# Performance work log

Hardware: AMD Instinct MI355X
Metric: run time of the kernel (lower is better)

## Reference

```python
import jax, jax.numpy as jnp
import numpy as np

C, H, V, N, T = 1024, 256, 10000, 16, 256


def setup_inputs() -> dict:
    key = jax.random.key(0)
    ks = jax.random.split(key, 16)
    s = 1.0 / np.sqrt(H)
    rn = lambda k, shape, sc: (jax.random.normal(k, shape, dtype=jnp.float32) * sc)
    d = {}
    d["text"] = jax.random.randint(ks[0], (N, T), 0, V)
    d["start_emb"] = rn(ks[1], (C, H), 1.0)
    d["sw1"] = rn(ks[2], (H, H), s); d["sb1"] = jnp.zeros((H,), jnp.float32)
    d["sw2"] = rn(ks[3], (H, H), s); d["sb2"] = jnp.zeros((H,), jnp.float32)
    d["sw3"] = rn(ks[4], (H, 1), s); d["sb3"] = jnp.zeros((1,), jnp.float32)
    d["state_emb"] = rn(ks[5], (C, H), 1.0)
    d["tw1"] = rn(ks[6], (H, H), s); d["tb1"] = jnp.zeros((H,), jnp.float32)
    d["tw2"] = rn(ks[7], (H, H), s); d["tb2"] = jnp.zeros((H,), jnp.float32)
    d["tw3"] = rn(ks[8], (H, C), s); d["tb3"] = jnp.zeros((C,), jnp.float32)
    d["pre_emb"] = rn(ks[9], (C, H), 1.0)
    d["ew1"] = rn(ks[10], (H, H), s); d["eb1"] = jnp.zeros((H,), jnp.float32)
    d["ew2"] = rn(ks[11], (H, H), s); d["eb2"] = jnp.zeros((H,), jnp.float32)
    d["ew3"] = rn(ks[12], (H, V), s); d["eb3"] = jnp.zeros((V,), jnp.float32)
    return d


def _res(x, w1, b1, w2, b2):
    # ResidualLayerOld: relu(lin2(relu(lin1(x)))) + x
    return jax.nn.relu(jax.nn.relu(x @ w1 + b1) @ w2 + b2) + x


def reference(text, start_emb, sw1, sb1, sw2, sb2, sw3, sb3,
              state_emb, tw1, tb1, tw2, tb2, tw3, tb3,
              pre_emb, ew1, eb1, ew2, eb2, ew3, eb3):
    # start: [C] log p(z_0)
    start = jax.nn.log_softmax((_res(start_emb, sw1, sb1, sw2, sb2) @ sw3 + sb3)[:, 0])
    # transition: log_softmax over next state, then permute -> [next, prev]
    trans = jax.nn.log_softmax(_res(state_emb, tw1, tb1, tw2, tb2) @ tw3 + tb3, axis=-1).T
    # emission: log_softmax over vocab, permute -> [V, C]
    emit = jax.nn.log_softmax(_res(pre_emb, ew1, eb1, ew2, eb2) @ ew3 + eb3, axis=-1).T

    obs = emit[text]                      # [N, T, C] log p(x_t | z_t=c)
    alpha0 = start[None, :] + obs[:, 0]   # [N, C]

    def step(alpha, e_t):
        # log-semiring matvec: alpha'[n,j] = logsumexp_i alpha[n,i] + trans[j,i]
        a = jax.scipy.special.logsumexp(alpha[:, None, :] + trans[None, :, :], axis=-1) + e_t
        return a, None

    alpha, _ = jax.lax.scan(step, alpha0, jnp.swapaxes(obs, 0, 1)[1:])
    # evidence: logsumexp over final states, summed over batch (full lengths)
    return jax.scipy.special.logsumexp(alpha, axis=-1).sum()
```

## Files before the change

kernel.cpp:

```cpp
#include <hip/hip_runtime.h>
#include <hip/hip_bf16.h>
#include <cstddef>

#define CC 1024
#define HH 256
#define VV 10000
#define NN 16
#define TT 256
#define NB 16

typedef __attribute__((ext_vector_type(8))) short s8b;
typedef __attribute__((ext_vector_type(4))) float f32x4;
typedef __attribute__((ext_vector_type(4))) unsigned int u32x4;

__device__ __forceinline__ unsigned short f2bf(float f) {
    unsigned int b = __builtin_bit_cast(unsigned int, f);
    b += 0x7FFFu + ((b >> 16) & 1u);
    return (unsigned short)(b >> 16);
}
__device__ __forceinline__ float bf2f(unsigned short u) {
    return __builtin_bit_cast(float, ((unsigned int)u) << 16);
}

struct ResArgs { const float *x, *w1, *b1, *w2, *b2; float* o; };
struct ResArgs3 { ResArgs a[3]; };

__global__ __launch_bounds__(256) void k_res(ResArgs3 A)
{
    ResArgs R = A.a[blockIdx.y];
    const int r0 = blockIdx.x * 16;
    const int th = threadIdx.x;
    __shared__ float xs[256][24];
    __shared__ float hs[256][24];
    #pragma unroll
    for (int k = 0; k < 16; k++) xs[th][k] = R.x[(size_t)(r0 + k) * HH + th];
    __syncthreads();
    float acc[16];
    float b1v = R.b1[th];
    #pragma unroll
    for (int r = 0; r < 16; r++) acc[r] = b1v;
    for (int h = 0; h < HH; h++) {
        float w = R.w1[(size_t)h * HH + th];
        #pragma unroll
        for (int r = 0; r < 16; r++) acc[r] = fmaf(xs[h][r], w, acc[r]);
    }
    #pragma unroll
    for (int r = 0; r < 16; r++) hs[th][r] = fmaxf(acc[r], 0.f);
    __syncthreads();
    float b2v = R.b2[th];
    #pragma unroll
    for (int r = 0; r < 16; r++) acc[r] = b2v;
    for (int h = 0; h < HH; h++) {
        float w = R.w2[(size_t)h * HH + th];
        #pragma unroll
        for (int r = 0; r < 16; r++) acc[r] = fmaf(hs[h][r], w, acc[r]);
    }
    #pragma unroll
    for (int r = 0; r < 16; r++) {
        size_t idx = (size_t)(r0 + r) * HH + th;
        R.o[idx] = fmaxf(acc[r], 0.f) + R.x[idx];
    }
}

__global__ __launch_bounds__(256) void k_slog(const float* __restrict__ res_s,
                                              const float* __restrict__ sw3,
                                              const float* __restrict__ sb3,
                                              float* __restrict__ slog)
{
    __shared__ float wv[256];
    const int th = threadIdx.x;
    const int c = blockIdx.x * 256 + th;
    wv[th] = sw3[th];
    __syncthreads();
    const float* row = res_s + (size_t)c * HH;
    float acc = 0.f;
    for (int h = 0; h < HH; h++) acc = fmaf(row[h], wv[h], acc);
    slog[c] = acc + sb3[0];
}

__global__ __launch_bounds__(256) void k_pt(const float* __restrict__ res_t,
                                            const float* __restrict__ tw3,
                                            const float* __restrict__ tb3,
                                            unsigned short* __restrict__ PB)
{
    const int r0 = blockIdx.x * 4;
    const int th = threadIdx.x;
    __shared__ float rs[4][256];
    __shared__ float sred[256];
    for (int k = 0; k < 4; k++) rs[k][th] = res_t[(size_t)(r0 + k) * HH + th];
    __syncthreads();
    float acc[4][4];
    #pragma unroll
    for (int r = 0; r < 4; r++)
        #pragma unroll
        for (int q = 0; q < 4; q++) acc[r][q] = tb3[th + q * 256];
    for (int h = 0; h < HH; h++) {
        float w0 = tw3[(size_t)h * CC + th];
        float w1 = tw3[(size_t)h * CC + th + 256];
        float w2 = tw3[(size_t)h * CC + th + 512];
        float w3 = tw3[(size_t)h * CC + th + 768];
        #pragma unroll
        for (int r = 0; r < 4; r++) {
            float xv = rs[r][h];
            acc[r][0] = fmaf(xv, w0, acc[r][0]);
            acc[r][1] = fmaf(xv, w1, acc[r][1]);
            acc[r][2] = fmaf(xv, w2, acc[r][2]);
            acc[r][3] = fmaf(xv, w3, acc[r][3]);
        }
    }
    for (int r = 0; r < 4; r++) {
        float m = fmaxf(fmaxf(acc[r][0], acc[r][1]), fmaxf(acc[r][2], acc[r][3]));
        sred[th] = m; __syncthreads();
        for (int off = 128; off > 0; off >>= 1) { if (th < off) sred[th] = fmaxf(sred[th], sred[th + off]); __syncthreads(); }
        float rm = sred[0]; __syncthreads();
        float ssum = __expf(acc[r][0] - rm) + __expf(acc[r][1] - rm) + __expf(acc[r][2] - rm) + __expf(acc[r][3] - rm);
        sred[th] = ssum; __syncthreads();
        for (int off = 128; off > 0; off >>= 1) { if (th < off) sred[th] += sred[th + off]; __syncthreads(); }
        float inv = 1.0f / sred[0]; __syncthreads();
        #pragma unroll
        for (int q = 0; q < 4; q++) {
            float p = __expf(acc[r][q] - rm) * inv;
            PB[(size_t)(th + q * 256) * CC + (r0 + r)] = f2bf(p);
        }
    }
}

__global__ __launch_bounds__(256) void k_emit(const float* __restrict__ res_e,
                                              const float* __restrict__ ew3,
                                              const float* __restrict__ eb3,
                                              unsigned short* __restrict__ emitT,
                                              float* __restrict__ epart)
{
    const int ct = blockIdx.x >> 2, jc = blockIdx.x & 3;
    const int c0 = ct * 16, j0 = jc * 2500;
    const int th = threadIdx.x;
    __shared__ float rs[256][24];
    __shared__ float sred[256];
    for (int k = 0; k < 16; k++) rs[th][k] = res_e[(size_t)(c0 + k) * HH + th];
    __syncthreads();
    float lm[16], ls[16];
    #pragma unroll
    for (int c = 0; c < 16; c++) { lm[c] = -1e30f; ls[c] = 0.f; }
    for (int it = 0; it < 10; it++) {
        int jo = it * 256 + th;
        if (jo < 2500) {
            int j = j0 + jo;
            float acc[16];
            float bb = eb3[j];
            #pragma unroll
            for (int c = 0; c < 16; c++) acc[c] = bb;
            for (int h = 0; h < HH; h++) {
                float wv = ew3[(size_t)h * VV + j];
                #pragma unroll
                for (int c = 0; c < 16; c++) acc[c] = fmaf(rs[h][c], wv, acc[c]);
            }
            #pragma unroll
            for (int c = 0; c < 16; c++) {
                emitT[(size_t)j * CC + c0 + c] = f2bf(acc[c]);
                float nm = fmaxf(lm[c], acc[c]);
                ls[c] = ls[c] * __expf(lm[c] - nm) + __expf(acc[c] - nm);
                lm[c] = nm;
            }
        }
    }
    for (int c = 0; c < 16; c++) {
        sred[th] = lm[c]; __syncthreads();
        for (int off = 128; off > 0; off >>= 1) { if (th < off) sred[th] = fmaxf(sred[th], sred[th + off]); __syncthreads(); }
        float gm = sred[0]; __syncthreads();
        sred[th] = (lm[c] > -1e29f) ? ls[c] * __expf(lm[c] - gm) : 0.f;
        __syncthreads();
        for (int off = 128; off > 0; off >>= 1) { if (th < off) sred[th] += sred[th + off]; __syncthreads(); }
        if (th == 0) {
            epart[((size_t)jc * CC + c0 + c) * 2]     = gm;
            epart[((size_t)jc * CC + c0 + c) * 2 + 1] = sred[0];
        }
        __syncthreads();
    }
}

__global__ __launch_bounds__(256) void k_lse(const float* __restrict__ epart,
                                             float* __restrict__ lse)
{
    int c = blockIdx.x * 256 + threadIdx.x;
    float M = -1e30f, S = 0.f;
    #pragma unroll
    for (int q = 0; q < 4; q++) {
        float m  = epart[((size_t)q * CC + c) * 2];
        float s2 = epart[((size_t)q * CC + c) * 2 + 1];
        float nm = fmaxf(M, m);
        S = S * __expf(M - nm) + s2 * __expf(m - nm);
        M = nm;
    }
    lse[c] = M + __logf(S);
}

__global__ __launch_bounds__(256) void k_eprob(unsigned short* __restrict__ emitT,
                                               const float* __restrict__ lse)
{
    __shared__ float ls[1024];
    const int th = threadIdx.x;
    for (int i = th; i < 1024; i += 256) ls[i] = lse[i];
    __syncthreads();
    size_t base = ((size_t)blockIdx.x * 256 + th) * 8;
    int c0 = (int)(base & 1023);
    s8b v = *(const s8b*)(emitT + base);
    unsigned short o[8];
    #pragma unroll
    for (int e = 0; e < 8; e++)
        o[e] = f2bf(__expf(bf2f((unsigned short)v[e]) - ls[c0 + e]));
    s8b ov;
    #pragma unroll
    for (int e = 0; e < 8; e++) ov[e] = (short)o[e];
    *(s8b*)(emitT + base) = ov;
}

__device__ __forceinline__ void load_stage(const unsigned short* vbuf_t, int th, char* vl)
{
    const unsigned short* sb = vbuf_t + th * 8;
    s8b ch[8];
    #pragma unroll
    for (int c = 0; c < 8; c++)
        asm volatile("global_load_dwordx4 %0, %1, off sc0 sc1"
                     : "=v"(ch[c]) : "v"(sb + c * 2048));
    asm volatile("s_waitcnt vmcnt(0)" ::: "memory");
    __builtin_amdgcn_sched_barrier(0);
    for (;;) {
        unsigned int miss = 0u;
        #pragma unroll
        for (int c = 0; c < 8; c++) {
            u32x4 d = __builtin_bit_cast(u32x4, ch[c]);
            if (d[0] == 0xFFFFFFFFu || d[1] == 0xFFFFFFFFu ||
                d[2] == 0xFFFFFFFFu || d[3] == 0xFFFFFFFFu) miss |= 1u << c;
        }
        if (miss == 0u) break;
        #pragma unroll
        for (int c = 0; c < 8; c++)
            if (miss & (1u << c))
                asm volatile("global_load_dwordx4 %0, %1, off sc0 sc1"
                             : "=v"(ch[c]) : "v"(sb + c * 2048));
        asm volatile("s_waitcnt vmcnt(0)" ::: "memory");
        __builtin_amdgcn_sched_barrier(0);
    }
    #pragma unroll
    for (int c = 0; c < 8; c++) {
        int ow = c * 4096 + th * 16;
        *(s8b*)(vl + (ow ^ (((ow >> 11) & 7) << 4))) = ch[c];
    }
}

__global__ void __launch_bounds__(256, 1) k_fwd(
    const unsigned short* __restrict__ PB,
    const unsigned short* __restrict__ eprob,
    const float* __restrict__ slog,
    const int* __restrict__ text,
    unsigned short* vbuf,
    float* __restrict__ outp)
{
    const int blk = blockIdx.x;
    const int th = threadIdx.x;
    const int w = th >> 6, l = th & 63;
    const int lhi = l >> 4, llo = l & 15;
    const int jglob = blk * 64 + w * 16 + llo;

    __shared__ int toks[NN * TT];
    __shared__ __align__(16) unsigned short vlds[NN * CC];
    __shared__ __align__(16) unsigned short vtile[16][72];
    __shared__ float swk[4];
    __shared__ float fin[16];

    for (int i = th; i < NN * TT; i += 256) toks[i] = text[i];

    s8b bfr[32];
    {
        const unsigned short* pbj = PB + (size_t)jglob * CC + lhi * 8;
        #pragma unroll
        for (int kt = 0; kt < 32; kt++)
            bfr[kt] = *(const s8b*)(pbj + kt * 32);
    }
    s8b ones;
    #pragma unroll
    for (int e = 0; e < 8; e++) ones[e] = (short)0x3F80;

    float x0 = slog[th], x1 = slog[th + 256], x2 = slog[th + 512], x3 = slog[th + 768];
    float mw = fmaxf(fmaxf(x0, x1), fmaxf(x2, x3));
    #pragma unroll
    for (int o = 32; o; o >>= 1) mw = fmaxf(mw, __shfl_xor(mw, o));
    __syncthreads();
    if (l == 0) swk[w] = mw;
    __syncthreads();
    float gm = fmaxf(fmaxf(swk[0], swk[1]), fmaxf(swk[2], swk[3]));
    __syncthreads();
    float e4 = __expf(x0 - gm) + __expf(x1 - gm) + __expf(x2 - gm) + __expf(x3 - gm);
    #pragma unroll
    for (int o = 32; o; o >>= 1) e4 += __shfl_xor(e4, o);
    if (l == 0) swk[w] = e4;
    __syncthreads();
    float slse = gm + __logf(swk[0] + swk[1] + swk[2] + swk[3]);
    __syncthreads();

    if (th < 64) {
        int jj = blk * 64 + th;
        float p0 = __expf(slog[jj] - slse);
        #pragma unroll
        for (int n = 0; n < 16; n++)
            vtile[n][th] = f2bf(p0 * bf2f(eprob[(size_t)toks[n * TT] * CC + jj]));
    }
    __syncthreads();
    if (th < 128) {
        int n = th >> 3, seg = th & 7;
        s8b val = *(const s8b*)&vtile[n][seg * 8];
        unsigned short* dst = vbuf + (size_t)n * CC + blk * 64 + seg * 8;
        asm volatile("global_store_dwordx4 %0, %1, off sc0 sc1" :: "v"(dst), "v"(val) : "memory");
    }

    float logaccq[4] = {0.f, 0.f, 0.f, 0.f};
    char* vl = (char*)vlds;
    const int rkey = (llo & 7) << 4;
    const int rbase = llo * 2048 + lhi * 16;

    for (int t = 1; t < TT; t++) {
        float epf[4];
        #pragma unroll
        for (int q = 0; q < 4; q++)
            epf[q] = bf2f(eprob[(size_t)toks[(lhi * 4 + q) * TT + t] * CC + jglob]);

        load_stage(vbuf + (size_t)(t - 1) * (NN * CC), th, vl);
        __syncthreads();

        f32x4 ac0 = {0,0,0,0}, ac1 = {0,0,0,0}, ac2 = {0,0,0,0}, ac3 = {0,0,0,0};
        f32x4 ao0 = {0,0,0,0}, ao1 = {0,0,0,0};
        #pragma unroll
        for (int kt = 0; kt < 32; kt += 4) {
            s8b a0 = *(const s8b*)(vl + ((rbase + (kt + 0) * 64) ^ rkey));
            s8b a1 = *(const s8b*)(vl + ((rbase + (kt + 1) * 64) ^ rkey));
            s8b a2 = *(const s8b*)(vl + ((rbase + (kt + 2) * 64) ^ rkey));
            s8b a3 = *(const s8b*)(vl + ((rbase + (kt + 3) * 64) ^ rkey));
            ac0 = __builtin_amdgcn_mfma_f32_16x16x32_bf16(a0, bfr[kt + 0], ac0, 0, 0, 0);
            ao0 = __builtin_amdgcn_mfma_f32_16x16x32_bf16(a0, ones,        ao0, 0, 0, 0);
            ac1 = __builtin_amdgcn_mfma_f32_16x16x32_bf16(a1, bfr[kt + 1], ac1, 0, 0, 0);
            ao1 = __builtin_amdgcn_mfma_f32_16x16x32_bf16(a1, ones,        ao1, 0, 0, 0);
            ac2 = __builtin_amdgcn_mfma_f32_16x16x32_bf16(a2, bfr[kt + 2], ac2, 0, 0, 0);
            ao0 = __builtin_amdgcn_mfma_f32_16x16x32_bf16(a2, ones,        ao0, 0, 0, 0);
            ac3 = __builtin_amdgcn_mfma_f32_16x16x32_bf16(a3, bfr[kt + 3], ac3, 0, 0, 0);
            ao1 = __builtin_amdgcn_mfma_f32_16x16x32_bf16(a3, ones,        ao1, 0, 0, 0);
        }
        f32x4 acc = (ac0 + ac1) + (ac2 + ac3);
        f32x4 aco = ao0 + ao1;

        #pragma unroll
        for (int q = 0; q < 4; q++) {
            float S = aco[q];
            logaccq[q] += __logf(S);
            float vq = acc[q] * (1.0f / S) * epf[q];
            vtile[lhi * 4 + q][w * 16 + llo] = f2bf(vq);
        }
        __syncthreads();

        if (th < 128) {
            int n = th >> 3, seg = th & 7;
            s8b val = *(const s8b*)&vtile[n][seg * 8];
            unsigned short* dst = vbuf + (size_t)t * (NN * CC) + (size_t)n * CC + blk * 64 + seg * 8;
            asm volatile("global_store_dwordx4 %0, %1, off sc0 sc1" :: "v"(dst), "v"(val) : "memory");
        }
    }

    if (blk == 0) {
        load_stage(vbuf + (size_t)255 * (NN * CC), th, vl);
        __syncthreads();
        f32x4 ao0 = {0,0,0,0}, ao1 = {0,0,0,0};
        #pragma unroll
        for (int kt = 0; kt < 32; kt += 2) {
            s8b a0 = *(const s8b*)(vl + ((rbase + (kt + 0) * 64) ^ rkey));
            s8b a1 = *(const s8b*)(vl + ((rbase + (kt + 1) * 64) ^ rkey));
            ao0 = __builtin_amdgcn_mfma_f32_16x16x32_bf16(a0, ones, ao0, 0, 0, 0);
            ao1 = __builtin_amdgcn_mfma_f32_16x16x32_bf16(a1, ones, ao1, 0, 0, 0);
        }
        f32x4 acoF = ao0 + ao1;
        if (w == 0 && llo == 0) {
            #pragma unroll
            for (int q = 0; q < 4; q++)
                fin[lhi * 4 + q] = logaccq[q] + __logf(acoF[q]);
        }
        __syncthreads();
        if (th == 0) {
            float tot = 0.f;
            for (int n = 0; n < 16; n++) tot += fin[n];
            outp[0] = tot;
        }
    }
}

extern "C" void kernel_launch(void* const* d_in, const int* in_sizes, int n_in,
                              void* d_out, int out_size, void* d_ws, size_t ws_size,
                              hipStream_t stream) {
    const int*   text      = (const int*)  d_in[0];
    const float* start_emb = (const float*)d_in[1];
    const float* sw1 = (const float*)d_in[2];
    const float* sb1 = (const float*)d_in[3];
    const float* sw2 = (const float*)d_in[4];
    const float* sb2 = (const float*)d_in[5];
    const float* sw3 = (const float*)d_in[6];
    const float* sb3 = (const float*)d_in[7];
    const float* state_emb = (const float*)d_in[8];
    const float* tw1 = (const float*)d_in[9];
    const float* tb1 = (const float*)d_in[10];
    const float* tw2 = (const float*)d_in[11];
    const float* tb2 = (const float*)d_in[12];
    const float* tw3 = (const float*)d_in[13];
    const float* tb3 = (const float*)d_in[14];
    const float* pre_emb = (const float*)d_in[15];
    const float* ew1 = (const float*)d_in[16];
    const float* eb1 = (const float*)d_in[17];
    const float* ew2 = (const float*)d_in[18];
    const float* eb2 = (const float*)d_in[19];
    const float* ew3 = (const float*)d_in[20];
    const float* eb3 = (const float*)d_in[21];

    char* wsp = (char*)d_ws;
    unsigned short* PB    = (unsigned short*)(wsp);
    unsigned short* emitT = (unsigned short*)(wsp + ((size_t)2 << 20));
    float* res_s = (float*)(wsp + ((size_t)2 << 20));
    float* res_t = (float*)(wsp + ((size_t)3 << 20));
    float* res_e = (float*)(wsp + 22577152u);
    float* slog  = (float*)(wsp + 23625728u);
    float* epart = (float*)(wsp + 23633920u);
    float* lse   = (float*)(wsp + 23666688u);
    unsigned short* vbuf = (unsigned short*)(wsp + ((size_t)23 << 20));
    float* outp  = (float*)d_out;

    if (ws_size < ((size_t)31 << 20)) return;

    hipMemsetAsync(vbuf, 0xFF, (size_t)TT * NN * CC * sizeof(unsigned short), stream);

    ResArgs3 ra;
    ra.a[0] = { start_emb, sw1, sb1, sw2, sb2, res_s };
    ra.a[1] = { state_emb, tw1, tb1, tw2, tb2, res_t };
    ra.a[2] = { pre_emb,   ew1, eb1, ew2, eb2, res_e };

    hipLaunchKernelGGL(k_res,   dim3(64, 3), dim3(256), 0, stream, ra);
    hipLaunchKernelGGL(k_slog,  dim3(4),     dim3(256), 0, stream, res_s, sw3, sb3, slog);
    hipLaunchKernelGGL(k_pt,    dim3(256),   dim3(256), 0, stream, res_t, tw3, tb3, PB);
    hipLaunchKernelGGL(k_emit,  dim3(256),   dim3(256), 0, stream, res_e, ew3, eb3, emitT, epart);
    hipLaunchKernelGGL(k_lse,   dim3(4),     dim3(256), 0, stream, epart, lse);
    hipLaunchKernelGGL(k_eprob, dim3(5000),  dim3(256), 0, stream, emitT, lse);
    hipLaunchKernelGGL(k_fwd,   dim3(NB),    dim3(256), 0, stream,
                       PB, emitT, slog, text, vbuf, outp);
}
```

Baseline: 1.121 ms.

## Compute emission logits with bf16 MFMA tiles and a finer vocab split

Replaces the scalar FP32 emission GEMM (1024x256 by 256x10000) with a kernel that stages swizzled bf16 tiles of res_e and ew3 in LDS and runs 16x16x32 bf16 MFMA instructions. The vocabulary is split into 40 blocks of 256 instead of 4 chunks, with per-block online max/sum partials reduced in k_lse. This targets the compute-bound scalar FMA loop and its low parallelism. The cost is bf16 rounding of the GEMM inputs and a more complex reduction, and the transposed global loads of ew3 are strided.

```diff
diff --git a/kernel.cpp b/kernel.cpp
--- a/kernel.cpp
+++ b/kernel.cpp
@@ -8,6 +8,7 @@
 #define NN 16
 #define TT 256
 #define NB 16
+#define NVB 40
 
 typedef __attribute__((ext_vector_type(8))) short s8b;
 typedef __attribute__((ext_vector_type(4))) float f32x4;
@@ -125,68 +126,150 @@
     }
 }
 
-__global__ __launch_bounds__(256) void k_emit(const float* __restrict__ res_e,
-                                              const float* __restrict__ ew3,
-                                              const float* __restrict__ eb3,
-                                              unsigned short* __restrict__ emitT,
-                                              float* __restrict__ epart)
-{
-    const int ct = blockIdx.x >> 2, jc = blockIdx.x & 3;
-    const int c0 = ct * 16, j0 = jc * 2500;
+__global__ __launch_bounds__(256) void k_emitg(const float* __restrict__ res_e,
+                                               const float* __restrict__ ew3,
+                                               const float* __restrict__ eb3,
+                                               unsigned short* __restrict__ emitT,
+                                               float* __restrict__ epart2)
+{
+    const int vb = blockIdx.x, c0 = blockIdx.y * 64;
     const int th = threadIdx.x;
-    __shared__ float rs[256][24];
-    __shared__ float sred[256];
-    for (int k = 0; k < 16; k++) rs[th][k] = res_e[(size_t)(c0 + k) * HH + th];
-    __syncthreads();
-    float lm[16], ls[16];
-    #pragma unroll
-    for (int c = 0; c < 16; c++) { lm[c] = -1e30f; ls[c] = 0.f; }
-    for (int it = 0; it < 10; it++) {
-        int jo = it * 256 + th;
-        if (jo < 2500) {
-            int j = j0 + jo;
-            float acc[16];
-            float bb = eb3[j];
+    const int w = th >> 6, l = th & 63;
+    const int lhi = l >> 4, llo = l & 15;
+    const int wv = w & 1, wc = w >> 1;
+
+    __shared__ __align__(16) unsigned short ewT[64 * 256];
+    __shared__ __align__(16) unsigned short rsb[64 * 256];
+    __shared__ float ebl[64];
+    __shared__ float wlse[4][2][16][2];
+
+    {
+        char* base = (char*)rsb;
+        #pragma unroll
+        for (int i = 0; i < 8; i++) {
+            int g = i * 2048 + th * 8;
+            int row = g >> 8, h0 = g & 255;
+            const float* src = res_e + (size_t)(c0 + row) * HH + h0;
+            float4 f0 = *(const float4*)(src);
+            float4 f1 = *(const float4*)(src + 4);
+            s8b pk;
+            pk[0] = (short)f2bf(f0.x); pk[1] = (short)f2bf(f0.y);
+            pk[2] = (short)f2bf(f0.z); pk[3] = (short)f2bf(f0.w);
+            pk[4] = (short)f2bf(f1.x); pk[5] = (short)f2bf(f1.y);
+            pk[6] = (short)f2bf(f1.z); pk[7] = (short)f2bf(f1.w);
+            *(s8b*)(base + row * 512 + ((h0 * 2) ^ ((row & 7) << 4))) = pk;
+        }
+    }
+
+    float rM[2] = {-1e30f, -1e30f}, rS[2] = {0.f, 0.f};
+
+    for (int r = 0; r < 4; r++) {
+        const int v0r = vb * 256 + r * 64;
+        __syncthreads();
+        {
+            int tv = th & 63;
+            char* base = (char*)ewT;
+            int rowoff = tv * 512;
+            int key = (tv & 7) << 4;
+            int vglob = v0r + tv;
+            bool valid = vglob < VV;
+            #pragma unroll 8
+            for (int i = 0; i < 64; i++) {
+                int h = (th >> 6) + i * 4;
+                float x = valid ? ew3[(size_t)h * VV + vglob] : 0.f;
+                *(unsigned short*)(base + rowoff + ((h * 2) ^ key)) = f2bf(x);
+            }
+        }
+        if (th < 64) ebl[th] = (v0r + th < VV) ? eb3[v0r + th] : 0.f;
+        __syncthreads();
+
+        f32x4 acc[2][2] = {{{0,0,0,0},{0,0,0,0}},{{0,0,0,0},{0,0,0,0}}};
+        const char* ea = (const char*)ewT;
+        const char* rb = (const char*)rsb;
+        const int arow0 = wv * 32 + llo, arow1 = wv * 32 + 16 + llo;
+        const int brow0 = wc * 32 + llo, brow1 = wc * 32 + 16 + llo;
+        const int akey0 = (arow0 & 7) << 4, akey1 = akey0;
+        const int bkey0 = (brow0 & 7) << 4;
+        #pragma unroll
+        for (int kt = 0; kt < 8; kt++) {
+            int off = kt * 64 + lhi * 16;
+            s8b a0 = *(const s8b*)(ea + arow0 * 512 + (off ^ akey0));
+            s8b a1 = *(const s8b*)(ea + arow1 * 512 + (off ^ akey1));
+            s8b b0 = *(const s8b*)(rb + brow0 * 512 + (off ^ bkey0));
+            s8b b1 = *(const s8b*)(rb + brow1 * 512 + (off ^ bkey0));
+            acc[0][0] = __builtin_amdgcn_mfma_f32_16x16x32_bf16(a0, b0, acc[0][0], 0, 0, 0);
+            acc[0][1] = __builtin_amdgcn_mfma_f32_16x16x32_bf16(a0, b1, acc[0][1], 0, 0, 0);
+            acc[1][0] = __builtin_amdgcn_mfma_f32_16x16x32_bf16(a1, b0, acc[1][0], 0, 0, 0);
+            acc[1][1] = __builtin_amdgcn_mfma_f32_16x16x32_bf16(a1, b1, acc[1][1], 0, 0, 0);
+        }
+
+        float um[2] = {-1e30f, -1e30f}, us[2] = {0.f, 0.f};
+        #pragma unroll
+        for (int u = 0; u < 2; u++) {
+            float vals[8];
             #pragma unroll
-            for (int c = 0; c < 16; c++) acc[c] = bb;
-            for (int h = 0; h < HH; h++) {
-                float wv = ew3[(size_t)h * VV + j];
+            for (int s = 0; s < 2; s++) {
                 #pragma unroll
-                for (int c = 0; c < 16; c++) acc[c] = fmaf(rs[h][c], wv, acc[c]);
+                for (int q = 0; q < 4; q++) {
+                    int vloc = wv * 32 + s * 16 + lhi * 4 + q;
+                    int vglob = v0r + vloc;
+                    float logit = acc[s][u][q] + ebl[vloc];
+                    bool valid = vglob < VV;
+                    if (valid)
+                        emitT[(size_t)vglob * CC + (c0 + wc * 32 + u * 16 + llo)] = f2bf(logit);
+                    vals[s * 4 + q] = valid ? logit : -1e30f;
+                }
             }
+            float m = vals[0];
             #pragma unroll
-            for (int c = 0; c < 16; c++) {
-                emitT[(size_t)j * CC + c0 + c] = f2bf(acc[c]);
-                float nm = fmaxf(lm[c], acc[c]);
-                ls[c] = ls[c] * __expf(lm[c] - nm) + __expf(acc[c] - nm);
-                lm[c] = nm;
+            for (int e = 1; e < 8; e++) m = fmaxf(m, vals[e]);
+            float ss = 0.f;
+            #pragma unroll
+            for (int e = 0; e < 8; e++) ss += __expf(vals[e] - m);
+            #pragma unroll
+            for (int o = 16; o < 64; o <<= 1) {
+                float m2 = __shfl_xor(m, o);
+                float s2 = __shfl_xor(ss, o);
+                float nm = fmaxf(m, m2);
+                ss = ss * __expf(m - nm) + s2 * __expf(m2 - nm);
+                m = nm;
             }
-        }
-    }
-    for (int c = 0; c < 16; c++) {
-        sred[th] = lm[c]; __syncthreads();
-        for (int off = 128; off > 0; off >>= 1) { if (th < off) sred[th] = fmaxf(sred[th], sred[th + off]); __syncthreads(); }
-        float gm = sred[0]; __syncthreads();
-        sred[th] = (lm[c] > -1e29f) ? ls[c] * __expf(lm[c] - gm) : 0.f;
-        __syncthreads();
-        for (int off = 128; off > 0; off >>= 1) { if (th < off) sred[th] += sred[th + off]; __syncthreads(); }
-        if (th == 0) {
-            epart[((size_t)jc * CC + c0 + c) * 2]     = gm;
-            epart[((size_t)jc * CC + c0 + c) * 2 + 1] = sred[0];
-        }
-        __syncthreads();
-    }
-}
-
-__global__ __launch_bounds__(256) void k_lse(const float* __restrict__ epart,
+            um[u] = m; us[u] = ss;
+        }
+        if (l < 16) {
+            #pragma unroll
+            for (int u = 0; u < 2; u++) {
+                wlse[w][u][l][0] = um[u];
+                wlse[w][u][l][1] = us[u];
+            }
+        }
+        __syncthreads();
+        if (th < 64) {
+            int wc2 = th >> 5, u2 = (th >> 4) & 1, ll2 = th & 15;
+            float m1 = wlse[2 * wc2][u2][ll2][0], s1 = wlse[2 * wc2][u2][ll2][1];
+            float m2 = wlse[2 * wc2 + 1][u2][ll2][0], s2 = wlse[2 * wc2 + 1][u2][ll2][1];
+            float nm = fmaxf(m1, m2);
+            float ns = s1 * __expf(m1 - nm) + s2 * __expf(m2 - nm);
+            float om = rM[0], os = rS[0];
+            float fm = fmaxf(om, nm);
+            rS[0] = os * __expf(om - fm) + ns * __expf(nm - fm);
+            rM[0] = fm;
+        }
+    }
+    if (th < 64) {
+        epart2[((size_t)vb * CC + c0 + th) * 2]     = rM[0];
+        epart2[((size_t)vb * CC + c0 + th) * 2 + 1] = rS[0];
+    }
+}
+
+__global__ __launch_bounds__(256) void k_lse(const float* __restrict__ epart2,
                                              float* __restrict__ lse)
 {
     int c = blockIdx.x * 256 + threadIdx.x;
     float M = -1e30f, S = 0.f;
-    #pragma unroll
-    for (int q = 0; q < 4; q++) {
-        float m  = epart[((size_t)q * CC + c) * 2];
-        float s2 = epart[((size_t)q * CC + c) * 2 + 1];
+    for (int vb = 0; vb < NVB; vb++) {
+        float m  = epart2[((size_t)vb * CC + c) * 2];
+        float s2 = epart2[((size_t)vb * CC + c) * 2 + 1];
         float nm = fmaxf(M, m);
         S = S * __expf(M - nm) + s2 * __expf(m - nm);
         M = nm;
@@ -423,8 +506,8 @@
     float* res_t = (float*)(wsp + ((size_t)3 << 20));
     float* res_e = (float*)(wsp + 22577152u);
     float* slog  = (float*)(wsp + 23625728u);
-    float* epart = (float*)(wsp + 23633920u);
-    float* lse   = (float*)(wsp + 23666688u);
+    float* lse   = (float*)(wsp + 23629824u);
+    float* epart2= (float*)(wsp + 23633920u);
     unsigned short* vbuf = (unsigned short*)(wsp + ((size_t)23 << 20));
     float* outp  = (float*)d_out;
 
@@ -437,12 +520,12 @@
     ra.a[1] = { state_emb, tw1, tb1, tw2, tb2, res_t };
     ra.a[2] = { pre_emb,   ew1, eb1, ew2, eb2, res_e };
 
-    hipLaunchKernelGGL(k_res,   dim3(64, 3), dim3(256), 0, stream, ra);
-    hipLaunchKernelGGL(k_slog,  dim3(4),     dim3(256), 0, stream, res_s, sw3, sb3, slog);
-    hipLaunchKernelGGL(k_pt,    dim3(256),   dim3(256), 0, stream, res_t, tw3, tb3, PB);
-    hipLaunchKernelGGL(k_emit,  dim3(256),   dim3(256), 0, stream, res_e, ew3, eb3, emitT, epart);
-    hipLaunchKernelGGL(k_lse,   dim3(4),     dim3(256), 0, stream, epart, lse);
-    hipLaunchKernelGGL(k_eprob, dim3(5000),  dim3(256), 0, stream, emitT, lse);
-    hipLaunchKernelGGL(k_fwd,   dim3(NB),    dim3(256), 0, stream,
+    hipLaunchKernelGGL(k_res,   dim3(64, 3),   dim3(256), 0, stream, ra);
+    hipLaunchKernelGGL(k_slog,  dim3(4),       dim3(256), 0, stream, res_s, sw3, sb3, slog);
+    hipLaunchKernelGGL(k_pt,    dim3(256),     dim3(256), 0, stream, res_t, tw3, tb3, PB);
+    hipLaunchKernelGGL(k_emitg, dim3(NVB, 16), dim3(256), 0, stream, res_e, ew3, eb3, emitT, epart2);
+    hipLaunchKernelGGL(k_lse,   dim3(4),       dim3(256), 0, stream, epart2, lse);
+    hipLaunchKernelGGL(k_eprob, dim3(5000),    dim3(256), 0, stream, emitT, lse);
+    hipLaunchKernelGGL(k_fwd,   dim3(NB),      dim3(256), 0, stream,
                        PB, emitT, slog, text, vbuf, outp);
 }
```

After: 979.3 us. 1.14x faster.
